# Performance work log

Measured on AMD Instinct MI355X. Metric: run time of the kernel, lower is better.

The kernel has to match this reference:

```python
import jax, jax.numpy as jnp
import numpy as np

B, S, D, H, DFF, E = 8, 1024, 1024, 16, 4096, 16
T = B * S
C = (2 * T) // E  # top-2 capacity, capacity_factor_eff = 1.0
EPS = 1.1920929e-07


def setup_inputs() -> dict:
    key = jax.random.key(0)
    ks = jax.random.split(key, 16)
    r = lambda k, shape, sc: jax.random.normal(k, shape, dtype=jnp.float32) * sc
    return {
        "x": r(ks[0], (B, S, D), 1.0),
        "in_proj_w": r(ks[1], (3 * D, D), 0.02),
        "in_proj_b": jnp.zeros((3 * D,), jnp.float32),
        "out_proj_w": r(ks[2], (D, D), 0.02),
        "out_proj_b": jnp.zeros((D,), jnp.float32),
        "ln1_g": jnp.ones((D,), jnp.float32),
        "ln1_b": jnp.zeros((D,), jnp.float32),
        "ln2_g": jnp.ones((D,), jnp.float32),
        "ln2_b": jnp.zeros((D,), jnp.float32),
        "wg": r(ks[3], (D, E), 0.02),
        "w1": r(ks[4], (E, D, DFF), 0.02),
        "b1": jnp.zeros((E, DFF), jnp.float32),
        "w2": r(ks[5], (E, DFF, D), 0.02),
        "b2": jnp.zeros((E, D), jnp.float32),
    }


def _layernorm(v, g, b):
    m = v.mean(-1, keepdims=True)
    var = ((v - m) ** 2).mean(-1, keepdims=True)
    return (v - m) * jax.lax.rsqrt(var + 1e-5) * g + b


def reference(x, in_proj_w, in_proj_b, out_proj_w, out_proj_b,
              ln1_g, ln1_b, ln2_g, ln2_b, wg, w1, b1, w2, b2):
    hd = D // H
    # ---- self-attention block (dropout=0, eval) ----
    qkv = x @ in_proj_w.T + in_proj_b          # [B,S,3D]
    q, k, v = jnp.split(qkv, 3, axis=-1)
    heads = lambda t: t.reshape(B, S, H, hd).transpose(0, 2, 1, 3)  # [B,H,S,hd]
    q, k, v = heads(q), heads(k), heads(v)
    att = jax.nn.softmax(jnp.einsum('bhqd,bhkd->bhqk', q, k) / np.float32(np.sqrt(hd)), axis=-1)
    o = jnp.einsum('bhqk,bhkd->bhqd', att, v).transpose(0, 2, 1, 3).reshape(B, S, D)
    o = o @ out_proj_w.T + out_proj_b
    x = _layernorm(x + o, ln1_g, ln1_b)
    # ---- top-2 MoE (GShard/deepspeed-style gating, no noise at eval) ----
    xt = x.reshape(T, D)
    logits = xt @ wg                                    # [T,E]
    gates = jax.nn.softmax(logits, axis=-1)
    idx1 = jnp.argmax(gates, axis=-1)
    m1 = jax.nn.one_hot(idx1, E, dtype=jnp.float32)
    logits2 = jnp.where(m1 > 0, -jnp.inf, logits)
    idx2 = jnp.argmax(logits2, axis=-1)
    m2 = jax.nn.one_hot(idx2, E, dtype=jnp.float32)
    loc1 = jnp.cumsum(m1, axis=0) - m1                  # position within expert for top-1
    loc2 = jnp.cumsum(m2, axis=0) - m2 + m1.sum(0, keepdims=True)
    m1 = m1 * (loc1 < C)                                # drop tokens over capacity
    m2 = m2 * (loc2 < C)
    p1 = (loc1 * m1).sum(-1).astype(jnp.int32)          # [T] capacity slot
    p2 = (loc2 * m2).sum(-1).astype(jnp.int32)
    g1 = (gates * m1).sum(-1)
    g2 = (gates * m2).sum(-1)
    denom = jnp.maximum(g1 + g2, EPS)
    g1, g2 = g1 / denom, g2 / denom
    keep1 = m1.sum(-1)                                  # 1.0 if kept else 0.0
    keep2 = m2.sum(-1)
    # dispatch: scatter tokens into [E, C, D] expert buffers
    buf = jnp.zeros((E, C, D), x.dtype)
    buf = buf.at[idx1, p1].add(xt * keep1[:, None]).at[idx2, p2].add(xt * keep2[:, None])
    # grouped expert FFN
    h = jax.nn.relu(jnp.einsum('ecd,edh->ech', buf, w1) + b1[:, None, :])
    y = jnp.einsum('ech,ehd->ecd', h, w2) + b2[:, None, :]
    # combine: gather back and weight by normalized gates (zero if dropped)
    moe_out = (g1 * keep1)[:, None] * y[idx1, p1] + (g2 * keep2)[:, None] * y[idx2, p2]
    x = _layernorm(x + moe_out.reshape(B, S, D), ln2_g, ln2_b)
    return x
```

## Files before the change

### kernel.cpp

```cpp
#include <hip/hip_runtime.h>
#include <cstdint>

#define DEVI __device__ __forceinline__

typedef short short8 __attribute__((ext_vector_type(8)));
typedef float f32x4 __attribute__((ext_vector_type(4)));
typedef unsigned short u16;
typedef u16 u16x4 __attribute__((ext_vector_type(4)));

static constexpr int Bz = 8, Ss = 1024, Dd = 1024, Hh = 16, HD = 64, DFF = 4096, Ee = 16;
static constexpr int Tt = Bz * Ss;
static constexpr int Cap = (2 * Tt) / Ee;
static constexpr int D3 = 3 * Dd;
static constexpr float EPSc = 1.1920929e-07f;
static constexpr size_t PT = (size_t)Tt * Dd;

DEVI u16 f2b(float f) {
    union { float f; uint32_t u; } v; v.f = f;
    return (u16)((v.u + 0x7FFFu + ((v.u >> 16) & 1u)) >> 16);
}
DEVI float b2f(u16 h) {
    union { uint32_t u; float f; } v; v.u = ((uint32_t)h) << 16; return v.f;
}
DEVI f32x4 zf4() { f32x4 v; v[0] = 0.f; v[1] = 0.f; v[2] = 0.f; v[3] = 0.f; return v; }

DEVI void gl16(const u16* g, u16* l) {
    __builtin_amdgcn_global_load_lds(
        (const __attribute__((address_space(1))) void*)g,
        (__attribute__((address_space(3))) void*)l, 16, 0, 0);
}

DEVI int swzb(int row, int col) {
    int byte = (row * 64 + col) * 2;
    byte ^= (row & 7) << 4;
    return byte >> 1;
}

__global__ __launch_bounds__(256)
void split3_kernel(const float* __restrict__ in, u16* __restrict__ out, long long n) {
    const long long i = ((long long)blockIdx.x * 256 + threadIdx.x) * 4;
    if (i >= n) return;
    const float4 v = *(const float4*)(in + i);
    const float f[4] = {v.x, v.y, v.z, v.w};
    u16x4 ph, pm, pl;
#pragma unroll
    for (int c = 0; c < 4; ++c) {
        const u16 hi = f2b(f[c]);
        const float r1 = f[c] - b2f(hi);
        const u16 mi = f2b(r1);
        const float r2 = r1 - b2f(mi);
        const u16 lo = f2b(r2);
        ph[c] = hi; pm[c] = mi; pl[c] = lo;
    }
    *(u16x4*)(out + i) = ph;
    *(u16x4*)(out + n + i) = pm;
    *(u16x4*)(out + 2 * n + i) = pl;
}

__global__ __launch_bounds__(256)
void tconv64_kernel(const float* __restrict__ in, u16* __restrict__ out, int R, int Cc) {
    __shared__ u16 tile[64][68];
    const int z = blockIdx.z;
    const int r0 = blockIdx.y * 64, c0 = blockIdx.x * 64;
    const int tr = threadIdx.x >> 4;
    const int tc4 = (threadIdx.x & 15) * 4;
    const float* ip = in + (size_t)z * R * Cc;
#pragma unroll
    for (int i = 0; i < 4; ++i) {
        const int row = tr + i * 16;
        const float4 v = *(const float4*)(ip + (size_t)(r0 + row) * Cc + c0 + tc4);
        u16x4 w;
        w[0] = f2b(v.x); w[1] = f2b(v.y); w[2] = f2b(v.z); w[3] = f2b(v.w);
        *(u16x4*)(&tile[row][tc4]) = w;
    }
    __syncthreads();
    u16* op = out + (size_t)z * R * Cc;
#pragma unroll
    for (int i = 0; i < 4; ++i) {
        const int orow = tr + i * 16;
        u16x4 w;
#pragma unroll
        for (int j = 0; j < 4; ++j) w[j] = tile[tc4 + j][orow];
        *(u16x4*)(op + (size_t)(c0 + orow) * R + r0 + tc4) = w;
    }
}

__global__ __launch_bounds__(256)
void vtrans_kernel(const u16* __restrict__ vh, const u16* __restrict__ vl,
                   u16* __restrict__ vth, u16* __restrict__ vtl) {
    __shared__ u16 th[32][33], tl[32][33];
    const int bh = blockIdx.z, d0 = blockIdx.y * 32, s0 = blockIdx.x * 32;
    const int bb = bh >> 4, hh = bh & 15;
    const int tr = threadIdx.x >> 5, tc = threadIdx.x & 31;
#pragma unroll
    for (int i = 0; i < 4; ++i) {
        const size_t src = (size_t)(bb * Ss + s0 + tr + i * 8) * Dd + hh * HD + d0 + tc;
        th[tr + i * 8][tc] = vh[src];
        tl[tr + i * 8][tc] = vl[src];
    }
    __syncthreads();
#pragma unroll
    for (int i = 0; i < 4; ++i) {
        const size_t dst = ((size_t)bh * HD + d0 + tr + i * 8) * Ss + s0 + tc;
        vth[dst] = th[tc][tr + i * 8];
        vtl[dst] = tl[tc][tr + i * 8];
    }
}

template <int SPLITS, int MODE>
__global__ __launch_bounds__(256)
void gemm_gl(const u16* __restrict__ A, const u16* __restrict__ Bt, void* __restrict__ Cout,
             const float* __restrict__ bias, int M, int N, int K,
             size_t psA, size_t psB,
             u16* __restrict__ qh, u16* __restrict__ ql,
             u16* __restrict__ kh, u16* __restrict__ kl,
             u16* __restrict__ vh, u16* __restrict__ vl) {
    __shared__ u16 As[SPLITS * 128 * 32];
    __shared__ u16 Bs[SPLITS * 128 * 32];
    const int tid = threadIdx.x;
    const int lane = tid & 63, wid = tid >> 6;
    const int wm = wid >> 1, wn = wid & 1;
    const int m0 = blockIdx.y * 128, n0 = blockIdx.x * 128;
    const int lr = lane & 15, lg = lane >> 4;
    const int lrow = lane >> 2;
    const int lcol = (lane & 3) * 8;

    f32x4 acc[4][4];
#pragma unroll
    for (int i = 0; i < 4; ++i)
#pragma unroll
        for (int j = 0; j < 4; ++j) acc[i][j] = zf4();

    for (int kt = 0; kt < K; kt += 32) {
#pragma unroll
        for (int p = 0; p < SPLITS; ++p) {
#pragma unroll
            for (int c = 0; c < 2; ++c) {
                const int r0 = wid * 32 + c * 16;
                gl16(A + p * psA + (size_t)(m0 + r0 + lrow) * K + kt + lcol,
                     As + p * 4096 + r0 * 32 + lane * 8);
                gl16(Bt + p * psB + (size_t)(n0 + r0 + lrow) * K + kt + lcol,
                     Bs + p * 4096 + r0 * 32 + lane * 8);
            }
        }
        __syncthreads();

        short8 af[SPLITS][4];
#pragma unroll
        for (int p = 0; p < SPLITS; ++p)
#pragma unroll
            for (int i = 0; i < 4; ++i)
                af[p][i] = *(const short8*)(As + p * 4096 + (wm * 64 + i * 16 + lr) * 32 + lg * 8);

#pragma unroll
        for (int bp = 0; bp < SPLITS; ++bp) {
            short8 bf[4];
#pragma unroll
            for (int j = 0; j < 4; ++j)
                bf[j] = *(const short8*)(Bs + bp * 4096 + (wn * 64 + j * 16 + lr) * 32 + lg * 8);
#pragma unroll
            for (int ap = 0; ap + bp < SPLITS; ++ap)
#pragma unroll
                for (int i = 0; i < 4; ++i)
#pragma unroll
                    for (int j = 0; j < 4; ++j)
                        acc[i][j] = __builtin_amdgcn_mfma_f32_16x16x32_bf16(af[ap][i], bf[j], acc[i][j], 0, 0, 0);
        }
        __syncthreads();
    }

    const int r4 = lg * 4;
    const int region = n0 >> 10;
#pragma unroll
    for (int j = 0; j < 4; ++j) {
        const int col = n0 + wn * 64 + j * 16 + lr;
        const float bv = bias[col];
#pragma unroll
        for (int i = 0; i < 4; ++i) {
#pragma unroll
            for (int r = 0; r < 4; ++r) {
                const int rowg = m0 + wm * 64 + i * 16 + r4 + r;
                float v = acc[i][j][r] + bv;
                if (MODE == 2) {
                    ((float*)Cout)[(size_t)rowg * N + col] = v;
                } else {
                    const size_t off = (size_t)rowg * Dd + (col & 1023);
                    if (region == 0) {
                        const float fs = v * 0.125f;
                        const u16 h = f2b(fs);
                        qh[off] = h; ql[off] = f2b(fs - b2f(h));
                    } else if (region == 1) {
                        const u16 h = f2b(v);
                        kh[off] = h; kl[off] = f2b(v - b2f(h));
                    } else {
                        const u16 h = f2b(v);
                        vh[off] = h; vl[off] = f2b(v - b2f(h));
                    }
                }
            }
        }
    }
}

template <int RELU>
__global__ __launch_bounds__(512)
void gemm_x2(const u16* __restrict__ A, const u16* __restrict__ Bt, u16* __restrict__ Cout,
             const float* __restrict__ bias, int M, int N, int K,
             size_t sA, size_t sB, size_t sC, int sBias) {
    __shared__ u16 lds[2][2][256 * 64];
    const int tid = threadIdx.x, lane = tid & 63, wid = tid >> 6;
    const int wm = wid >> 2, wn = wid & 3;
    const int lr = lane & 15, lg = lane >> 4;
    const int m0 = blockIdx.y * 256, n0 = blockIdx.x * 256;
    const int e = blockIdx.z;
    const u16* Ab = A + (size_t)e * sA;
    const u16* Bb = Bt + (size_t)e * sB;

    const int srow = wid * 8 + (lane >> 3);
    const int scol = (lane & 7) * 8;

    f32x4 acc[8][4];
#pragma unroll
    for (int i = 0; i < 8; ++i)
#pragma unroll
        for (int j = 0; j < 4; ++j) acc[i][j] = zf4();

#define STAGE_X2(b, kt)                                                              \
    {                                                                                \
        _Pragma("unroll")                                                            \
        for (int c = 0; c < 4; ++c)                                                  \
            gl16(Ab + (size_t)(m0 + c * 64 + srow) * K + (kt) + scol,                \
                 &lds[b][0][(c * 64 + srow) * 64 + scol]);                           \
        _Pragma("unroll")                                                            \
        for (int c = 0; c < 4; ++c)                                                  \
            gl16(Bb + (size_t)(n0 + c * 64 + srow) * K + (kt) + scol,                \
                 &lds[b][1][(c * 64 + srow) * 64 + scol]);                           \
    }

#define COMPUTE_X2(b)                                                                \
    {                                                                                \
        _Pragma("unroll")                                                            \
        for (int ks = 0; ks < 2; ++ks) {                                             \
            short8 af[8], bf[4];                                                     \
            _Pragma("unroll")                                                        \
            for (int i = 0; i < 8; ++i)                                              \
                af[i] = *(const short8*)(&lds[b][0][(wm * 128 + i * 16 + lr) * 64 + ks * 32 + lg * 8]); \
            _Pragma("unroll")                                                        \
            for (int j = 0; j < 4; ++j)                                              \
                bf[j] = *(const short8*)(&lds[b][1][(wn * 64 + j * 16 + lr) * 64 + ks * 32 + lg * 8]);  \
            _Pragma("unroll")                                                        \
            for (int i = 0; i < 8; ++i)                                              \
                _Pragma("unroll")                                                    \
                for (int j = 0; j < 4; ++j)                                          \
                    acc[i][j] = __builtin_amdgcn_mfma_f32_16x16x32_bf16(af[i], bf[j], acc[i][j], 0, 0, 0); \
        }                                                                            \
    }

    const int nt = K >> 6;
    STAGE_X2(0, 0)
    for (int t = 0; t < nt - 1; ++t) {
        const int cur = t & 1;
        STAGE_X2(cur ^ 1, (t + 1) * 64)
        asm volatile("s_waitcnt vmcnt(8)" ::: "memory");
        __builtin_amdgcn_s_barrier();
        COMPUTE_X2(cur)
        asm volatile("s_waitcnt lgkmcnt(0)" ::: "memory");
        __builtin_amdgcn_s_barrier();
    }
    asm volatile("s_waitcnt vmcnt(0)" ::: "memory");
    __builtin_amdgcn_s_barrier();
    COMPUTE_X2((nt - 1) & 1)

#undef STAGE_X2
#undef COMPUTE_X2

    const int r4 = lg * 4;
#pragma unroll
    for (int j = 0; j < 4; ++j) {
        const int col = n0 + wn * 64 + j * 16 + lr;
        const float bv = bias[(size_t)e * sBias + col];
#pragma unroll
        for (int i = 0; i < 8; ++i) {
#pragma unroll
            for (int r = 0; r < 4; ++r) {
                const int rowg = m0 + wm * 128 + i * 16 + r4 + r;
                float v = acc[i][j][r] + bv;
                if (RELU) v = fmaxf(v, 0.f);
                Cout[(size_t)e * sC + (size_t)rowg * N + col] = f2b(v);
            }
        }
    }
}

__global__ __launch_bounds__(256)
void attn_mfma(const u16* __restrict__ qhp, const u16* __restrict__ qlp,
               const u16* __restrict__ khp, const u16* __restrict__ klp,
               const u16* __restrict__ vthp, const u16* __restrict__ vtlp,
               u16* __restrict__ os) {
    __shared__ u16 Khi[64 * 64], Klo[64 * 64];
    __shared__ u16 Vhi[64 * 64], Vlo[64 * 64];
    __shared__ u16 Phi[4][16 * 64], Plo[4][16 * 64];

    const int qt = blockIdx.x, bh = blockIdx.y;
    const int bb = bh >> 4, hh = bh & 15;
    const int tid = threadIdx.x, lane = tid & 63, wid = tid >> 6;
    const int lr = lane & 15, lg = lane >> 4;

    short8 qhi[2], qlo[2];
    {
        const size_t qbase = (size_t)(bb * Ss + qt * 64 + wid * 16 + lr) * Dd + hh * HD;
#pragma unroll
        for (int ks = 0; ks < 2; ++ks) {
            qhi[ks] = *(const short8*)(qhp + qbase + ks * 32 + lg * 8);
            qlo[ks] = *(const short8*)(qlp + qbase + ks * 32 + lg * 8);
        }
    }

    float mrun[4], lrun[4];
    f32x4 oacc[4];
#pragma unroll
    for (int r = 0; r < 4; ++r) { mrun[r] = -1e30f; lrun[r] = 0.f; }
#pragma unroll
    for (int nf = 0; nf < 4; ++nf) oacc[nf] = zf4();

    const int srow = tid >> 2;
    const int sd = (tid & 3) * 16;

    u16* const PhiW = Phi[wid];
    u16* const PloW = Plo[wid];

    for (int kt = 0; kt < Ss / 64; ++kt) {
        const size_t krow = (size_t)(bb * Ss + kt * 64 + srow) * Dd + hh * HD + sd;
        const short8 k0 = *(const short8*)(khp + krow);
        const short8 k1 = *(const short8*)(khp + krow + 8);
        const short8 l0 = *(const short8*)(klp + krow);
        const short8 l1 = *(const short8*)(klp + krow + 8);
        const size_t vrow = ((size_t)bh * HD + srow) * Ss + kt * 64 + sd;
        const short8 v0 = *(const short8*)(vthp + vrow);
        const short8 v1 = *(const short8*)(vthp + vrow + 8);
        const short8 w0 = *(const short8*)(vtlp + vrow);
        const short8 w1 = *(const short8*)(vtlp + vrow + 8);
        __syncthreads();
        *(short8*)(Khi + swzb(srow, sd)) = k0;
        *(short8*)(Khi + swzb(srow, sd + 8)) = k1;
        *(short8*)(Klo + swzb(srow, sd)) = l0;
        *(short8*)(Klo + swzb(srow, sd + 8)) = l1;
        *(short8*)(Vhi + swzb(srow, sd)) = v0;
        *(short8*)(Vhi + swzb(srow, sd + 8)) = v1;
        *(short8*)(Vlo + swzb(srow, sd)) = w0;
        *(short8*)(Vlo + swzb(srow, sd + 8)) = w1;
        __syncthreads();

        f32x4 sc[4];
#pragma unroll
        for (int nf = 0; nf < 4; ++nf) sc[nf] = zf4();
#pragma unroll
        for (int nf = 0; nf < 4; ++nf)
#pragma unroll
            for (int ks = 0; ks < 2; ++ks) {
                const short8 kh = *(const short8*)(Khi + swzb(nf * 16 + lr, ks * 32 + lg * 8));
                const short8 kl = *(const short8*)(Klo + swzb(nf * 16 + lr, ks * 32 + lg * 8));
                sc[nf] = __builtin_amdgcn_mfma_f32_16x16x32_bf16(qhi[ks], kh, sc[nf], 0, 0, 0);
                sc[nf] = __builtin_amdgcn_mfma_f32_16x16x32_bf16(qhi[ks], kl, sc[nf], 0, 0, 0);
                sc[nf] = __builtin_amdgcn_mfma_f32_16x16x32_bf16(qlo[ks], kh, sc[nf], 0, 0, 0);
                sc[nf] = __builtin_amdgcn_mfma_f32_16x16x32_bf16(qlo[ks], kl, sc[nf], 0, 0, 0);
            }

        float scl[4];
#pragma unroll
        for (int r = 0; r < 4; ++r) {
            float m = fmaxf(fmaxf(sc[0][r], sc[1][r]), fmaxf(sc[2][r], sc[3][r]));
            m = fmaxf(m, __shfl_xor(m, 1));
            m = fmaxf(m, __shfl_xor(m, 2));
            m = fmaxf(m, __shfl_xor(m, 4));
            m = fmaxf(m, __shfl_xor(m, 8));
            const float mn = fmaxf(mrun[r], m);
            scl[r] = __expf(mrun[r] - mn);
            mrun[r] = mn;
            float s = 0.f;
#pragma unroll
            for (int nf = 0; nf < 4; ++nf) {
                const float p = __expf(sc[nf][r] - mn);
                sc[nf][r] = p;
                s += p;
            }
            s += __shfl_xor(s, 1);
            s += __shfl_xor(s, 2);
            s += __shfl_xor(s, 4);
            s += __shfl_xor(s, 8);
            lrun[r] = lrun[r] * scl[r] + s;
        }

#pragma unroll
        for (int nf = 0; nf < 4; ++nf)
#pragma unroll
            for (int r = 0; r < 4; ++r) {
                const float p = sc[nf][r];
                const u16 h = f2b(p);
                const int idx = swzb(lg * 4 + r, nf * 16 + lr);
                PhiW[idx] = h;
                PloW[idx] = f2b(p - b2f(h));
            }

#pragma unroll
        for (int nf = 0; nf < 4; ++nf)
#pragma unroll
            for (int r = 0; r < 4; ++r) oacc[nf][r] *= scl[r];

#pragma unroll
        for (int ks = 0; ks < 2; ++ks) {
            const short8 ph = *(const short8*)(PhiW + swzb(lr, ks * 32 + lg * 8));
            const short8 pl = *(const short8*)(PloW + swzb(lr, ks * 32 + lg * 8));
#pragma unroll
            for (int nf = 0; nf < 4; ++nf) {
                const short8 vh = *(const short8*)(Vhi + swzb(nf * 16 + lr, ks * 32 + lg * 8));
                const short8 vl = *(const short8*)(Vlo + swzb(nf * 16 + lr, ks * 32 + lg * 8));
                oacc[nf] = __builtin_amdgcn_mfma_f32_16x16x32_bf16(ph, vh, oacc[nf], 0, 0, 0);
                oacc[nf] = __builtin_amdgcn_mfma_f32_16x16x32_bf16(ph, vl, oacc[nf], 0, 0, 0);
                oacc[nf] = __builtin_amdgcn_mfma_f32_16x16x32_bf16(pl, vh, oacc[nf], 0, 0, 0);
                oacc[nf] = __builtin_amdgcn_mfma_f32_16x16x32_bf16(pl, vl, oacc[nf], 0, 0, 0);
            }
        }
    }

#pragma unroll
    for (int r = 0; r < 4; ++r) {
        const float inv = 1.f / lrun[r];
        const size_t base = (size_t)(bb * Ss + qt * 64 + wid * 16 + lg * 4 + r) * Dd + hh * HD;
#pragma unroll
        for (int nf = 0; nf < 4; ++nf) {
            const float o = oacc[nf][r] * inv;
            const u16 h = f2b(o);
            const float r1 = o - b2f(h);
            const u16 m = f2b(r1);
            const u16 l = f2b(r1 - b2f(m));
            const size_t off = base + nf * 16 + lr;
            os[off] = h;
            os[PT + off] = m;
            os[2 * PT + off] = l;
        }
    }
}

DEVI double block_reduce_d(double v, double* sred, int tid) {
#pragma unroll
    for (int off = 32; off > 0; off >>= 1) v += __shfl_down(v, off);
    __syncthreads();
    if ((tid & 63) == 0) sred[tid >> 6] = v;
    __syncthreads();
    return sred[0] + sred[1] + sred[2] + sred[3];
}

__global__ __launch_bounds__(256)
void ln1_kernel(const float* __restrict__ x, const float* __restrict__ ap,
                const float* __restrict__ g, const float* __restrict__ b,
                float* __restrict__ x1f) {
    __shared__ double sred[4];
    const int t = blockIdx.x, tid = threadIdx.x;
    const float4 xv = ((const float4*)(x + (size_t)t * Dd))[tid];
    const float4 av = ((const float4*)(ap + (size_t)t * Dd))[tid];
    const double v0 = (double)xv.x + (double)av.x;
    const double v1 = (double)xv.y + (double)av.y;
    const double v2 = (double)xv.z + (double)av.z;
    const double v3 = (double)xv.w + (double)av.w;
    const double s = block_reduce_d(v0 + v1 + v2 + v3, sred, tid);
    const double mean = s * (1.0 / Dd);
    const double c0 = v0 - mean, c1 = v1 - mean, c2 = v2 - mean, c3 = v3 - mean;
    const double s2 = block_reduce_d(c0 * c0 + c1 * c1 + c2 * c2 + c3 * c3, sred, tid);
    const double rstd = 1.0 / sqrt(s2 * (1.0 / Dd) + 1e-5);
    const float4 gv = ((const float4*)g)[tid];
    const float4 bv = ((const float4*)b)[tid];
    float4 ov;
    ov.x = (float)(c0 * rstd * (double)gv.x + (double)bv.x);
    ov.y = (float)(c1 * rstd * (double)gv.y + (double)bv.y);
    ov.z = (float)(c2 * rstd * (double)gv.z + (double)bv.z);
    ov.w = (float)(c3 * rstd * (double)gv.w + (double)bv.w);
    ((float4*)(x1f + (size_t)t * Dd))[tid] = ov;
}

__global__ __launch_bounds__(256)
void gate1_kernel(const float* __restrict__ x1f, const float* __restrict__ wg,
                  int* __restrict__ idx1, int* __restrict__ idx2,
                  float* __restrict__ gate1, float* __restrict__ gate2) {
    const int tid = threadIdx.x, lane = tid & 63, wid = tid >> 6;
    const int t = blockIdx.x * 4 + wid;
    double acc[16];
#pragma unroll
    for (int e = 0; e < 16; ++e) acc[e] = 0.0;
    for (int i = 0; i < 16; ++i) {
        const int d = i * 64 + lane;
        const double xv = (double)x1f[(size_t)t * Dd + d];
        const float4* wr = (const float4*)(wg + (size_t)d * 16);
        const float4 w0 = wr[0], w1 = wr[1], w2 = wr[2], w3 = wr[3];
        acc[0] += xv * (double)w0.x;  acc[1] += xv * (double)w0.y;
        acc[2] += xv * (double)w0.z;  acc[3] += xv * (double)w0.w;
        acc[4] += xv * (double)w1.x;  acc[5] += xv * (double)w1.y;
        acc[6] += xv * (double)w1.z;  acc[7] += xv * (double)w1.w;
        acc[8] += xv * (double)w2.x;  acc[9] += xv * (double)w2.y;
        acc[10] += xv * (double)w2.z; acc[11] += xv * (double)w2.w;
        acc[12] += xv * (double)w3.x; acc[13] += xv * (double)w3.y;
        acc[14] += xv * (double)w3.z; acc[15] += xv * (double)w3.w;
    }
#pragma unroll
    for (int e = 0; e < 16; ++e) {
        acc[e] += __shfl_xor(acc[e], 1);
        acc[e] += __shfl_xor(acc[e], 2);
        acc[e] += __shfl_xor(acc[e], 4);
        acc[e] += __shfl_xor(acc[e], 8);
        acc[e] += __shfl_xor(acc[e], 16);
        acc[e] += __shfl_xor(acc[e], 32);
    }
    if (lane == 0) {
        double mx = acc[0];
#pragma unroll
        for (int e = 1; e < 16; ++e) mx = fmax(mx, acc[e]);
        double z = 0.0, ex[16];
#pragma unroll
        for (int e = 0; e < 16; ++e) { ex[e] = exp(acc[e] - mx); z += ex[e]; }
        int b1 = 0; double v1 = acc[0];
#pragma unroll
        for (int e = 1; e < 16; ++e) if (acc[e] > v1) { v1 = acc[e]; b1 = e; }
        int b2 = (b1 == 0) ? 1 : 0; double v2 = acc[b2];
#pragma unroll
        for (int e = 0; e < 16; ++e) if (e != b1 && acc[e] > v2) { v2 = acc[e]; b2 = e; }
        const double rz = 1.0 / z;
        idx1[t] = b1; idx2[t] = b2;
        gate1[t] = (float)(ex[b1] * rz); gate2[t] = (float)(ex[b2] * rz);
    }
}

__global__ __launch_bounds__(256)
void gate2_kernel(const int* __restrict__ idx1, const int* __restrict__ idx2,
                  const float* __restrict__ gate1, const float* __restrict__ gate2,
                  int* __restrict__ p1, int* __restrict__ p2,
                  int* __restrict__ k1, int* __restrict__ k2,
                  float* __restrict__ w1, float* __restrict__ w2) {
    __shared__ int hist[16];
    __shared__ unsigned long long sb1[4][16], sb2[4][16];
    __shared__ int sbase1[16], sbase2[16];
    const int tid = threadIdx.x, lane = tid & 63, wid = tid >> 6;
    if (tid < 16) hist[tid] = 0;
    __syncthreads();
    for (int t = tid; t < Tt; t += 256) atomicAdd(&hist[idx1[t]], 1);
    __syncthreads();
    if (tid < 16) { sbase1[tid] = 0; sbase2[tid] = hist[tid]; }
    __syncthreads();
    const unsigned long long below = (1ULL << lane) - 1ULL;
    for (int ch = 0; ch < Tt / 256; ++ch) {
        const int t = ch * 256 + tid;
        const int a = idx1[t], b = idx2[t];
#pragma unroll
        for (int e = 0; e < 16; ++e) {
            const unsigned long long m1 = __ballot(a == e);
            const unsigned long long m2 = __ballot(b == e);
            if (lane == 0) { sb1[wid][e] = m1; sb2[wid][e] = m2; }
        }
        __syncthreads();
        int r1 = __popcll(sb1[wid][a] & below);
        int r2 = __popcll(sb2[wid][b] & below);
#pragma unroll
        for (int w = 0; w < 4; ++w)
            if (w < wid) { r1 += __popcll(sb1[w][a]); r2 += __popcll(sb2[w][b]); }
        const int loc1 = sbase1[a] + r1, loc2 = sbase2[b] + r2;
        const int kk1 = loc1 < Cap, kk2 = loc2 < Cap;
        const float g1 = kk1 ? gate1[t] : 0.f;
        const float g2 = kk2 ? gate2[t] : 0.f;
        const float dn = fmaxf(g1 + g2, EPSc);
        p1[t] = kk1 ? loc1 : 0;
        p2[t] = kk2 ? loc2 : 0;
        k1[t] = kk1; k2[t] = kk2;
        w1[t] = g1 / dn; w2[t] = g2 / dn;
        __syncthreads();
        if (tid == 0) {
#pragma unroll
            for (int e = 0; e < 16; ++e) {
                int c1 = 0, c2 = 0;
#pragma unroll
                for (int w = 0; w < 4; ++w) { c1 += __popcll(sb1[w][e]); c2 += __popcll(sb2[w][e]); }
                sbase1[e] += c1; sbase2[e] += c2;
            }
        }
        __syncthreads();
    }
}

__global__ __launch_bounds__(256)
void dispatch_kernel(const float* __restrict__ x1f,
                     const int* __restrict__ i1, const int* __restrict__ p1, const int* __restrict__ k1,
                     const int* __restrict__ i2, const int* __restrict__ p2, const int* __restrict__ k2,
                     u16* __restrict__ buf) {
    const int t = blockIdx.x, tid = threadIdx.x;
    const float4 v = ((const float4*)(x1f + (size_t)t * Dd))[tid];
    u16x4 pw;
    pw[0] = f2b(v.x); pw[1] = f2b(v.y); pw[2] = f2b(v.z); pw[3] = f2b(v.w);
    if (k1[t]) *(u16x4*)(buf + ((size_t)i1[t] * Cap + p1[t]) * Dd + tid * 4) = pw;
    if (k2[t]) *(u16x4*)(buf + ((size_t)i2[t] * Cap + p2[t]) * Dd + tid * 4) = pw;
}

__global__ __launch_bounds__(256)
void combine_ln2(const float* __restrict__ x1f, const u16* __restrict__ y,
                 const int* __restrict__ i1, const int* __restrict__ p1, const float* __restrict__ w1,
                 const int* __restrict__ i2, const int* __restrict__ p2, const float* __restrict__ w2,
                 const float* __restrict__ g, const float* __restrict__ b,
                 float* __restrict__ out) {
    __shared__ double sred[4];
    const int t = blockIdx.x, tid = threadIdx.x;
    const size_t r1 = ((size_t)i1[t] * Cap + p1[t]) * Dd;
    const size_t r2 = ((size_t)i2[t] * Cap + p2[t]) * Dd;
    const double a1 = (double)w1[t], a2 = (double)w2[t];
    const u16x4 y1 = *(const u16x4*)(y + r1 + tid * 4);
    const u16x4 y2 = *(const u16x4*)(y + r2 + tid * 4);
    const float4 xv = ((const float4*)(x1f + (size_t)t * Dd))[tid];
    const double v0 = (double)xv.x + a1 * (double)b2f(y1[0]) + a2 * (double)b2f(y2[0]);
    const double v1 = (double)xv.y + a1 * (double)b2f(y1[1]) + a2 * (double)b2f(y2[1]);
    const double v2 = (double)xv.z + a1 * (double)b2f(y1[2]) + a2 * (double)b2f(y2[2]);
    const double v3 = (double)xv.w + a1 * (double)b2f(y1[3]) + a2 * (double)b2f(y2[3]);
    const double s = block_reduce_d(v0 + v1 + v2 + v3, sred, tid);
    const double mean = s * (1.0 / Dd);
    const double c0 = v0 - mean, c1 = v1 - mean, c2 = v2 - mean, c3 = v3 - mean;
    const double s2 = block_reduce_d(c0 * c0 + c1 * c1 + c2 * c2 + c3 * c3, sred, tid);
    const double rstd = 1.0 / sqrt(s2 * (1.0 / Dd) + 1e-5);
    const float4 gv = ((const float4*)g)[tid];
    const float4 bv = ((const float4*)b)[tid];
    float4 ov;
    ov.x = (float)(c0 * rstd * (double)gv.x + (double)bv.x);
    ov.y = (float)(c1 * rstd * (double)gv.y + (double)bv.y);
    ov.z = (float)(c2 * rstd * (double)gv.z + (double)bv.z);
    ov.w = (float)(c3 * rstd * (double)gv.w + (double)bv.w);
    ((float4*)(out + (size_t)t * Dd))[tid] = ov;
}

extern "C" void kernel_launch(void* const* d_in, const int* in_sizes, int n_in,
                              void* d_out, int out_size, void* d_ws, size_t ws_size,
                              hipStream_t stream) {
    (void)in_sizes; (void)n_in; (void)out_size; (void)ws_size;
    const float* x    = (const float*)d_in[0];
    const float* inW  = (const float*)d_in[1];
    const float* inB  = (const float*)d_in[2];
    const float* outW = (const float*)d_in[3];
    const float* outB = (const float*)d_in[4];
    const float* ln1g = (const float*)d_in[5];
    const float* ln1b = (const float*)d_in[6];
    const float* ln2g = (const float*)d_in[7];
    const float* ln2b = (const float*)d_in[8];
    const float* wg   = (const float*)d_in[9];
    const float* w1   = (const float*)d_in[10];
    const float* b1   = (const float*)d_in[11];
    const float* w2   = (const float*)d_in[12];
    const float* b2   = (const float*)d_in[13];
    float* out = (float*)d_out;

    char* ws = (char*)d_ws;
    const size_t MB = 1024 * 1024;
    u16*   xs3   = (u16*)(ws + 0);
    u16*   inW3  = (u16*)(ws + 48 * MB);
    u16*   qh    = (u16*)(ws + 66 * MB);
    u16*   ql    = (u16*)(ws + 82 * MB);
    u16*   kh    = (u16*)(ws + 98 * MB);
    u16*   kl    = (u16*)(ws + 114 * MB);
    u16*   vh    = (u16*)(ws + 130 * MB);
    u16*   vl    = (u16*)(ws + 146 * MB);
    u16*   vth   = (u16*)(ws + 162 * MB);
    u16*   vtl   = (u16*)(ws + 178 * MB);
    u16*   os3   = (u16*)(ws + 194 * MB);
    u16*   outW3 = (u16*)(ws + 0);
    float* aproj = (float*)(ws + 6 * MB);
    u16*   wt    = (u16*)(ws + 0);
    u16*   hbuf  = (u16*)(ws + 128 * MB);
    u16*   ybuf  = (u16*)(ws + 256 * MB);
    u16*   ebuf  = (u16*)(ws + 288 * MB);
    float* x1f   = (float*)(ws + 320 * MB);
    char*  gbase = ws + 352 * MB;
    int*   idx1 = (int*)(gbase + 0 * Tt * 4);
    int*   idx2 = (int*)(gbase + 1 * Tt * 4);
    float* gt1  = (float*)(gbase + 2 * Tt * 4);
    float* gt2  = (float*)(gbase + 3 * Tt * 4);
    int*   p1   = (int*)(gbase + 4 * Tt * 4);
    int*   p2   = (int*)(gbase + 5 * Tt * 4);
    int*   k1   = (int*)(gbase + 6 * Tt * 4);
    int*   k2   = (int*)(gbase + 7 * Tt * 4);
    float* w1c  = (float*)(gbase + 8 * Tt * 4);
    float* w2c  = (float*)(gbase + 9 * Tt * 4);

    const long long nTD = (long long)Tt * Dd;
    const long long nW1 = (long long)D3 * Dd;
    const long long nW2 = (long long)Dd * Dd;

    split3_kernel<<<(int)(nTD / 1024), 256, 0, stream>>>(x, xs3, nTD);
    split3_kernel<<<(int)(nW1 / 1024), 256, 0, stream>>>(inW, inW3, nW1);
    gemm_gl<3, 3><<<dim3(D3 / 128, Tt / 128, 1), 256, 0, stream>>>(
        xs3, inW3, nullptr, inB, Tt, D3, Dd, (size_t)nTD, (size_t)nW1,
        qh, ql, kh, kl, vh, vl);
    vtrans_kernel<<<dim3(Ss / 32, HD / 32, Bz * Hh), 256, 0, stream>>>(vh, vl, vth, vtl);
    attn_mfma<<<dim3(Ss / 64, Bz * Hh), 256, 0, stream>>>(qh, ql, kh, kl, vth, vtl, os3);
    split3_kernel<<<(int)(nW2 / 1024), 256, 0, stream>>>(outW, outW3, nW2);
    gemm_gl<3, 2><<<dim3(Dd / 128, Tt / 128, 1), 256, 0, stream>>>(
        os3, outW3, aproj, outB, Tt, Dd, Dd, (size_t)nTD, (size_t)nW2,
        nullptr, nullptr, nullptr, nullptr, nullptr, nullptr);
    ln1_kernel<<<Tt, 256, 0, stream>>>(x, aproj, ln1g, ln1b, x1f);
    gate1_kernel<<<Tt / 4, 256, 0, stream>>>(x1f, wg, idx1, idx2, gt1, gt2);
    gate2_kernel<<<1, 256, 0, stream>>>(idx1, idx2, gt1, gt2, p1, p2, k1, k2, w1c, w2c);
    hipMemsetAsync(ebuf, 0, (size_t)Ee * Cap * Dd * 2, stream);
    dispatch_kernel<<<Tt, 256, 0, stream>>>(x1f, idx1, p1, k1, idx2, p2, k2, ebuf);
    tconv64_kernel<<<dim3(DFF / 64, Dd / 64, Ee), 256, 0, stream>>>(w1, wt, Dd, DFF);
    gemm_x2<1><<<dim3(DFF / 256, Cap / 256, Ee), 512, 0, stream>>>(
        ebuf, wt, hbuf, b1, Cap, DFF, Dd,
        (size_t)Cap * Dd, (size_t)DFF * Dd, (size_t)Cap * DFF, DFF);
    tconv64_kernel<<<dim3(Dd / 64, DFF / 64, Ee), 256, 0, stream>>>(w2, wt, DFF, Dd);
    gemm_x2<0><<<dim3(Dd / 256, Cap / 256, Ee), 512, 0, stream>>>(
        hbuf, wt, ybuf, b2, Cap, Dd, DFF,
        (size_t)Cap * DFF, (size_t)Dd * DFF, (size_t)Cap * Dd, Dd);
    combine_ln2<<<Tt, 256, 0, stream>>>(x1f, ybuf, idx1, p1, w1c, idx2, p2, w2c, ln2g, ln2b, out);
}
```

Before: 1.367 ms.

## Swizzle GEMM LDS tiles, prefetch attention K/V, parallelize routing base update

The GEMM kernel now XOR-swizzles the global source column per row while keeping the LDS destination linear. The fragment reads apply the matching XOR, which is meant to remove LDS bank conflicts when loading MFMA operands. The attention kernel register-prefetches the next K/V tile after the LDS store so global latency overlaps with compute, at the cost of more registers. The routing kernel spreads the per-expert base update across 16 threads instead of one.

Result: faster. 1.281 ms (-6.2%).

```diff
diff --git a/kernel.cpp b/kernel.cpp
--- a/kernel.cpp
+++ b/kernel.cpp
@@ -217,7 +217,7 @@
     const u16* Bb = Bt + (size_t)e * sB;
 
     const int srow = wid * 8 + (lane >> 3);
-    const int scol = (lane & 7) * 8;
+    const int sscol = (((lane & 7) ^ ((lane >> 3) & 7))) * 8;
 
     f32x4 acc[8][4];
 #pragma unroll
@@ -229,12 +229,12 @@
     {                                                                                \
         _Pragma("unroll")                                                            \
         for (int c = 0; c < 4; ++c)                                                  \
-            gl16(Ab + (size_t)(m0 + c * 64 + srow) * K + (kt) + scol,                \
-                 &lds[b][0][(c * 64 + srow) * 64 + scol]);                           \
+            gl16(Ab + (size_t)(m0 + c * 64 + srow) * K + (kt) + sscol,               \
+                 &lds[b][0][(c * 64 + srow) * 64 + (lane & 7) * 8]);                 \
         _Pragma("unroll")                                                            \
         for (int c = 0; c < 4; ++c)                                                  \
-            gl16(Bb + (size_t)(n0 + c * 64 + srow) * K + (kt) + scol,                \
-                 &lds[b][1][(c * 64 + srow) * 64 + scol]);                           \
+            gl16(Bb + (size_t)(n0 + c * 64 + srow) * K + (kt) + sscol,               \
+                 &lds[b][1][(c * 64 + srow) * 64 + (lane & 7) * 8]);                 \
     }
 
 #define COMPUTE_X2(b)                                                                \
@@ -244,10 +244,12 @@
             short8 af[8], bf[4];                                                     \
             _Pragma("unroll")                                                        \
             for (int i = 0; i < 8; ++i)                                              \
-                af[i] = *(const short8*)(&lds[b][0][(wm * 128 + i * 16 + lr) * 64 + ks * 32 + lg * 8]); \
+                af[i] = *(const short8*)(&lds[b][0][(wm * 128 + i * 16 + lr) * 64 +  \
+                                                    (((ks * 4 + lg) ^ (lr & 7)) * 8)]); \
             _Pragma("unroll")                                                        \
             for (int j = 0; j < 4; ++j)                                              \
-                bf[j] = *(const short8*)(&lds[b][1][(wn * 64 + j * 16 + lr) * 64 + ks * 32 + lg * 8]);  \
+                bf[j] = *(const short8*)(&lds[b][1][(wn * 64 + j * 16 + lr) * 64 +   \
+                                                    (((ks * 4 + lg) ^ (lr & 7)) * 8)]); \
             _Pragma("unroll")                                                        \
             for (int i = 0; i < 8; ++i)                                              \
                 _Pragma("unroll")                                                    \
@@ -329,27 +331,44 @@
     u16* const PhiW = Phi[wid];
     u16* const PloW = Plo[wid];
 
+    short8 ck0, ck1, cl0, cl1, cv0, cv1, cw0, cw1;
+    {
+        const size_t krow = (size_t)(bb * Ss + srow) * Dd + hh * HD + sd;
+        const size_t vrow = ((size_t)bh * HD + srow) * Ss + sd;
+        ck0 = *(const short8*)(khp + krow);
+        ck1 = *(const short8*)(khp + krow + 8);
+        cl0 = *(const short8*)(klp + krow);
+        cl1 = *(const short8*)(klp + krow + 8);
+        cv0 = *(const short8*)(vthp + vrow);
+        cv1 = *(const short8*)(vthp + vrow + 8);
+        cw0 = *(const short8*)(vtlp + vrow);
+        cw1 = *(const short8*)(vtlp + vrow + 8);
+    }
+
     for (int kt = 0; kt < Ss / 64; ++kt) {
-        const size_t krow = (size_t)(bb * Ss + kt * 64 + srow) * Dd + hh * HD + sd;
-        const short8 k0 = *(const short8*)(khp + krow);
-        const short8 k1 = *(const short8*)(khp + krow + 8);
-        const short8 l0 = *(const short8*)(klp + krow);
-        const short8 l1 = *(const short8*)(klp + krow + 8);
-        const size_t vrow = ((size_t)bh * HD + srow) * Ss + kt * 64 + sd;
-        const short8 v0 = *(const short8*)(vthp + vrow);
-        const short8 v1 = *(const short8*)(vthp + vrow + 8);
-        const short8 w0 = *(const short8*)(vtlp + vrow);
-        const short8 w1 = *(const short8*)(vtlp + vrow + 8);
         __syncthreads();
-        *(short8*)(Khi + swzb(srow, sd)) = k0;
-        *(short8*)(Khi + swzb(srow, sd + 8)) = k1;
-        *(short8*)(Klo + swzb(srow, sd)) = l0;
-        *(short8*)(Klo + swzb(srow, sd + 8)) = l1;
-        *(short8*)(Vhi + swzb(srow, sd)) = v0;
-        *(short8*)(Vhi + swzb(srow, sd + 8)) = v1;
-        *(short8*)(Vlo + swzb(srow, sd)) = w0;
-        *(short8*)(Vlo + swzb(srow, sd + 8)) = w1;
+        *(short8*)(Khi + swzb(srow, sd)) = ck0;
+        *(short8*)(Khi + swzb(srow, sd + 8)) = ck1;
+        *(short8*)(Klo + swzb(srow, sd)) = cl0;
+        *(short8*)(Klo + swzb(srow, sd + 8)) = cl1;
+        *(short8*)(Vhi + swzb(srow, sd)) = cv0;
+        *(short8*)(Vhi + swzb(srow, sd + 8)) = cv1;
+        *(short8*)(Vlo + swzb(srow, sd)) = cw0;
+        *(short8*)(Vlo + swzb(srow, sd + 8)) = cw1;
         __syncthreads();
+
+        if (kt < Ss / 64 - 1) {
+            const size_t krow = (size_t)(bb * Ss + (kt + 1) * 64 + srow) * Dd + hh * HD + sd;
+            const size_t vrow = ((size_t)bh * HD + srow) * Ss + (kt + 1) * 64 + sd;
+            ck0 = *(const short8*)(khp + krow);
+            ck1 = *(const short8*)(khp + krow + 8);
+            cl0 = *(const short8*)(klp + krow);
+            cl1 = *(const short8*)(klp + krow + 8);
+            cv0 = *(const short8*)(vthp + vrow);
+            cv1 = *(const short8*)(vthp + vrow + 8);
+            cw0 = *(const short8*)(vtlp + vrow);
+            cw1 = *(const short8*)(vtlp + vrow + 8);
+        }
 
         f32x4 sc[4];
 #pragma unroll
@@ -571,14 +590,12 @@
         k1[t] = kk1; k2[t] = kk2;
         w1[t] = g1 / dn; w2[t] = g2 / dn;
         __syncthreads();
-        if (tid == 0) {
-#pragma unroll
-            for (int e = 0; e < 16; ++e) {
-                int c1 = 0, c2 = 0;
-#pragma unroll
-                for (int w = 0; w < 4; ++w) { c1 += __popcll(sb1[w][e]); c2 += __popcll(sb2[w][e]); }
-                sbase1[e] += c1; sbase2[e] += c2;
-            }
+        if (tid < 16) {
+            const int e = tid;
+            int c1 = 0, c2 = 0;
+#pragma unroll
+            for (int w = 0; w < 4; ++w) { c1 += __popcll(sb1[w][e]); c2 += __popcll(sb2[w][e]); }
+            sbase1[e] += c1; sbase2[e] += c2;
         }
         __syncthreads();
     }
```
